# Kernel tuning notes

Measured on AMD Instinct MI355X. Metric: run time of the kernel, lower is better.

Reference implementation:

```python
import jax, jax.numpy as jnp
import numpy as np

LN_EPS = 1e-5
NORM_EPS = 1e-12
TEMPERATURE = 0.5


def _project(h, W1, b1, W2, b2, g, beta):
    # projection head: Linear -> ReLU -> Linear -> LayerNorm, then L2 normalize
    x = jnp.maximum(h @ W1 + b1, 0.0) @ W2 + b2          # [B, P]
    mu = jnp.mean(x, axis=-1, keepdims=True)
    var = jnp.mean(jnp.square(x - mu), axis=-1, keepdims=True)
    x = (x - mu) * jax.lax.rsqrt(var + LN_EPS) * g + beta
    n = jnp.linalg.norm(x, axis=-1, keepdims=True)
    return x / jnp.maximum(n, NORM_EPS)                   # [B, P]


def setup_inputs() -> dict:
    key = jax.random.key(0)
    ks = jax.random.split(key, 8)
    B, H, P, K, NBUF = 16384, 2048, 256, 64, 2000
    Hh = H // 2
    return {
        "hidden_states": jax.random.normal(ks[0], (B, H), jnp.float32),
        "positive_hidden": jax.random.normal(ks[1], (B, H), jnp.float32),
        "neg_buffer": jax.random.normal(ks[2], (NBUF, P), jnp.float32),
        "W1": jax.random.normal(ks[3], (H, Hh), jnp.float32) * (1.0 / np.sqrt(H)),
        "b1": jnp.zeros((Hh,), jnp.float32),
        "W2": jax.random.normal(ks[4], (Hh, P), jnp.float32) * (1.0 / np.sqrt(Hh)),
        "b2": jnp.zeros((P,), jnp.float32),
        "ln_gamma": jnp.ones((P,), jnp.float32),
        "ln_beta": jnp.zeros((P,), jnp.float32),
        "neg_indices": jax.random.randint(ks[5], (B, K), 0, NBUF, jnp.int32),
    }


def reference(hidden_states, positive_hidden, neg_buffer, W1, b1, W2, b2,
              ln_gamma, ln_beta, neg_indices):
    anchors = _project(hidden_states, W1, b1, W2, b2, ln_gamma, ln_beta)      # [B,P]
    positives = _project(positive_hidden, W1, b1, W2, b2, ln_gamma, ln_beta)  # [B,P]
    # negatives are detached in the original (buffer stores .detach() features)
    negs = jax.lax.stop_gradient(neg_buffer)[neg_indices]                      # [B,K,P]
    pos_sim = jnp.einsum('bp,bp->b', anchors, positives) / TEMPERATURE        # [B]
    neg_sims = jnp.einsum('bkp,bp->bk', negs, anchors) / TEMPERATURE          # [B,K]
    logits = jnp.concatenate([pos_sim[:, None], neg_sims], axis=1)            # [B,1+K]
    # cross-entropy with label 0 for every anchor, averaged over the batch
    loss = -jnp.mean(jax.nn.log_softmax(logits, axis=-1)[:, 0])
    return loss
```

## Files before the change

kernel.cpp:

```cpp
#include <hip/hip_runtime.h>
#include <hip/hip_bf16.h>
#include <cstdint>

#define BATCH   16384
#define HDIM    2048
#define HHDIM   1024
#define PDIM    256
#define KNEG    64
#define NBUF    2000
#define M1      (2 * BATCH)

typedef float  f32x4  __attribute__((ext_vector_type(4)));
typedef __bf16 bf16x8 __attribute__((ext_vector_type(8)));

typedef __attribute__((address_space(3))) unsigned int       lds_u32;
typedef __attribute__((address_space(1))) const unsigned int glb_u32;

__device__ __forceinline__ void gload_lds16(const void* g, void* l) {
  __builtin_amdgcn_global_load_lds((glb_u32*)g, (lds_u32*)l, 16, 0, 0);
}

#define VMCNT(n) asm volatile("s_waitcnt vmcnt(" #n ")" ::: "memory")

__global__ __launch_bounds__(256)
void cast_bf16_kernel(const float* __restrict__ src, __bf16* __restrict__ dst,
                      long n8) {
  long i = (long)blockIdx.x * blockDim.x + threadIdx.x;
  long stride = (long)gridDim.x * blockDim.x;
  for (; i < n8; i += stride) {
    f32x4 a = ((const f32x4*)src)[2 * i];
    f32x4 b = ((const f32x4*)src)[2 * i + 1];
    bf16x8 w;
    for (int j = 0; j < 4; ++j) { w[j] = (__bf16)a[j]; w[4 + j] = (__bf16)b[j]; }
    ((bf16x8*)dst)[i] = w;
  }
}

__global__ void transpose_cast_kernel(const float* __restrict__ src,
                                      __bf16* __restrict__ dst, int K, int N) {
  __shared__ float tile[32][33];
  int bn = blockIdx.x * 32, bk = blockIdx.y * 32;
  int tx = threadIdx.x, ty = threadIdx.y;
  for (int j = 0; j < 32; j += 8)
    tile[ty + j][tx] = src[(size_t)(bk + ty + j) * N + bn + tx];
  __syncthreads();
  for (int j = 0; j < 32; j += 8)
    dst[(size_t)(bn + ty + j) * K + bk + tx] = (__bf16)tile[tx][ty + j];
}

template <int KD, int BMH, int NBt, bool RELU_OUT, bool LNFUSE, int GRID>
__global__ __launch_bounds__(512)
void gemm_8ph(const __bf16* __restrict__ A, const __bf16* __restrict__ Bt,
              const float* __restrict__ bias,
              const float* __restrict__ lng, const float* __restrict__ lnb,
              void* __restrict__ Cv) {
  static_assert(!LNFUSE || NBt == 1, "LN fusion needs full rows per block");
  constexpr int KT    = KD / 64;
  constexpr int MI    = BMH / 32;
  constexpr int AHALF = BMH * 64;
  constexpr int BHALF = 128 * 64;
  constexpr int ASTEP = 2 * AHALF;
  constexpr int BSTEP = 2 * BHALF;
  constexpr int NDIM  = NBt * 256;
  constexpr int AUL   = BMH / 64;

  __shared__ __bf16 lA[2 * ASTEP];
  __shared__ __bf16 lB[2 * BSTEP];

  constexpr int Q = GRID / 8;
  int bid = blockIdx.x;
  int swb = (bid & 7) * Q + (bid >> 3);
  const int mb = swb / NBt, nb = swb % NBt;
  const long mrow0 = (long)mb * (2 * BMH);
  const int  ncol0 = nb * 256;

  const int tid = threadIdx.x;
  const int wid = tid >> 6, lane = tid & 63;
  const int wr = wid >> 2, wc = wid & 3;
  const int fl = lane & 15, fh = lane >> 4;

  int aoff[MI][2], boff[2][2];
  #pragma unroll
  for (int mi = 0; mi < MI; ++mi)
    #pragma unroll
    for (int ks = 0; ks < 2; ++ks) {
      int row = wr * (BMH / 2) + mi * 16 + fl;
      aoff[mi][ks] = row * 64 + (((ks * 4 + fh) ^ (row & 7)) * 8);
    }
  #pragma unroll
  for (int ni = 0; ni < 2; ++ni)
    #pragma unroll
    for (int ks = 0; ks < 2; ++ks) {
      int row = wc * 32 + ni * 16 + fl;
      boff[ni][ks] = row * 64 + (((ks * 4 + fh) ^ (row & 7)) * 8);
    }

  const int r0 = tid >> 3, sl = tid & 7;
  long aS[2][AUL], bS[2][2];
  #pragma unroll
  for (int h = 0; h < 2; ++h) {
    #pragma unroll
    for (int i = 0; i < AUL; ++i) {
      int rr = r0 + i * 64;
      int ss = sl ^ (rr & 7);
      aS[h][i] = (mrow0 + h * BMH + rr) * (long)KD + ss * 8;
    }
    #pragma unroll
    for (int i = 0; i < 2; ++i) {
      int rr = r0 + i * 64;
      int ss = sl ^ (rr & 7);
      bS[h][i] = ((long)(ncol0 + h * 128 + rr)) * KD + ss * 8;
    }
  }
  const int dstw = wid * 512;

  auto stA = [&](int h, int t) {
    __bf16* base = lA + (t & 1) * ASTEP + h * AHALF + dstw;
    #pragma unroll
    for (int i = 0; i < AUL; ++i)
      gload_lds16(A + aS[h][i] + (long)t * 64, (void*)(base + i * 4096));
  };
  auto stB = [&](int h, int t) {
    __bf16* base = lB + (t & 1) * BSTEP + h * BHALF + dstw;
    #pragma unroll
    for (int i = 0; i < 2; ++i)
      gload_lds16(Bt + bS[h][i] + (long)t * 64, (void*)(base + i * 4096));
  };

  bf16x8 aregA[MI][2], aregB[MI][2], breg0[2][2], breg1[2][2];
  auto loadA = [&](bf16x8 (&ar)[MI][2], int mh, int s) {
    const __bf16* base = lA + (s & 1) * ASTEP + mh * AHALF;
    #pragma unroll
    for (int mi = 0; mi < MI; ++mi)
      #pragma unroll
      for (int ks = 0; ks < 2; ++ks)
        ar[mi][ks] = *(const bf16x8*)(base + aoff[mi][ks]);
  };
  auto loadB = [&](bf16x8 (&br)[2][2], int nh, int s) {
    const __bf16* base = lB + (s & 1) * BSTEP + nh * BHALF;
    #pragma unroll
    for (int ni = 0; ni < 2; ++ni)
      #pragma unroll
      for (int ks = 0; ks < 2; ++ks)
        br[ni][ks] = *(const bf16x8*)(base + boff[ni][ks]);
  };

  f32x4 acc[2][2][MI][2] = {};

#define PHASE_MFMA(mh, nh, AR, BR)                                            \
  __builtin_amdgcn_s_setprio(1);                                              \
  _Pragma("unroll")                                                           \
  for (int ks = 0; ks < 2; ++ks) {                                            \
    _Pragma("unroll")                                                         \
    for (int mi = 0; mi < MI; ++mi) {                                         \
      _Pragma("unroll")                                                       \
      for (int ni = 0; ni < 2; ++ni)                                          \
        acc[mh][nh][mi][ni] = __builtin_amdgcn_mfma_f32_16x16x32_bf16(        \
            AR[mi][ks], BR[ni][ks], acc[mh][nh][mi][ni], 0, 0, 0);            \
    }                                                                         \
  }                                                                           \
  __builtin_amdgcn_s_setprio(0);

  stA(0, 0); stB(0, 0); stA(1, 0); stB(1, 0);
  stA(0, 1); stB(1, 1); stB(0, 1); stA(1, 1);
  if constexpr (AUL == 2) { VMCNT(8); } else { VMCNT(6); }
  __builtin_amdgcn_s_barrier();
  __builtin_amdgcn_sched_barrier(0);
  loadA(aregA, 0, 0);
  loadB(breg0, 0, 0);

  for (int s = 0; s < KT; ++s) {
    if (s >= 1 && s + 1 < KT) stB(0, s + 1);
    loadB(breg1, 1, s);
    PHASE_MFMA(0, 0, aregA, breg0);
    if (s + 1 < KT) {
      if constexpr (AUL == 2) { VMCNT(6); } else { VMCNT(5); }
    } else {
      VMCNT(0);
    }
    __builtin_amdgcn_s_barrier();
    __builtin_amdgcn_sched_barrier(0);

    if (s >= 1 && s + 1 < KT) stA(1, s + 1);
    loadA(aregB, 1, s);
    PHASE_MFMA(0, 1, aregA, breg1);
    __builtin_amdgcn_s_barrier();
    __builtin_amdgcn_sched_barrier(0);

    if (s + 2 < KT) stA(0, s + 2);
    PHASE_MFMA(1, 1, aregB, breg1);
    if (s + 2 < KT) {
      if constexpr (AUL == 2) { VMCNT(4); } else { VMCNT(2); }
    } else if (s + 1 < KT) {
      if constexpr (AUL == 2) { VMCNT(2); } else { VMCNT(1); }
    } else {
      VMCNT(0);
    }
    __builtin_amdgcn_s_barrier();
    __builtin_amdgcn_sched_barrier(0);

    if (s + 2 < KT) stB(1, s + 2);
    PHASE_MFMA(1, 0, aregB, breg0);
    if (s + 1 < KT) {
      loadA(aregA, 0, s + 1);
      loadB(breg0, 0, s + 1);
    }
    __builtin_amdgcn_s_barrier();
    __builtin_amdgcn_sched_barrier(0);
  }

#undef PHASE_MFMA

  if constexpr (LNFUSE) {
    float (*s1p)[4] = (float(*)[4])((float*)lA);
    float (*s2p)[4] = (float(*)[4])((float*)lA + 512);
    float (*n2p)[4] = (float(*)[4])((float*)lA + 1024);

    float v[2][2][MI][2][4];
    float gg[2][2], bb[2][2];
    #pragma unroll
    for (int nh = 0; nh < 2; ++nh)
      #pragma unroll
      for (int ni = 0; ni < 2; ++ni) {
        int c = nh * 128 + wc * 32 + ni * 16 + fl;
        float bv = bias[c];
        gg[nh][ni] = lng[c]; bb[nh][ni] = lnb[c];
        #pragma unroll
        for (int mh = 0; mh < 2; ++mh)
          #pragma unroll
          for (int mi = 0; mi < MI; ++mi)
            #pragma unroll
            for (int r = 0; r < 4; ++r)
              v[mh][nh][mi][ni][r] = acc[mh][nh][mi][ni][r] + bv;
      }

    #pragma unroll
    for (int mh = 0; mh < 2; ++mh)
      #pragma unroll
      for (int mi = 0; mi < MI; ++mi)
        #pragma unroll
        for (int r = 0; r < 4; ++r) {
          float s1 = 0.0f, s2 = 0.0f;
          #pragma unroll
          for (int nh = 0; nh < 2; ++nh)
            #pragma unroll
            for (int ni = 0; ni < 2; ++ni) {
              float x = v[mh][nh][mi][ni][r];
              s1 += x; s2 += x * x;
            }
          for (int m = 1; m < 16; m <<= 1) {
            s1 += __shfl_xor(s1, m, 64);
            s2 += __shfl_xor(s2, m, 64);
          }
          if (fl == 0) {
            int lr = mh * 64 + wr * 32 + mi * 16 + fh * 4 + r;
            s1p[lr][wc] = s1; s2p[lr][wc] = s2;
          }
        }
    __syncthreads();

    float n2loc[2][MI][4];
    #pragma unroll
    for (int mh = 0; mh < 2; ++mh)
      #pragma unroll
      for (int mi = 0; mi < MI; ++mi)
        #pragma unroll
        for (int r = 0; r < 4; ++r) {
          int lr = mh * 64 + wr * 32 + mi * 16 + fh * 4 + r;
          float t1 = s1p[lr][0] + s1p[lr][1] + s1p[lr][2] + s1p[lr][3];
          float t2 = s2p[lr][0] + s2p[lr][1] + s2p[lr][2] + s2p[lr][3];
          float mu = t1 * (1.0f / PDIM);
          float var = t2 * (1.0f / PDIM) - mu * mu;
          float rstd = rsqrtf(var + 1e-5f);
          float n2 = 0.0f;
          #pragma unroll
          for (int nh = 0; nh < 2; ++nh)
            #pragma unroll
            for (int ni = 0; ni < 2; ++ni) {
              float y = (v[mh][nh][mi][ni][r] - mu) * rstd * gg[nh][ni] + bb[nh][ni];
              v[mh][nh][mi][ni][r] = y;
              n2 += y * y;
            }
          for (int m = 1; m < 16; m <<= 1) n2 += __shfl_xor(n2, m, 64);
          n2loc[mh][mi][r] = n2;
        }
    #pragma unroll
    for (int mh = 0; mh < 2; ++mh)
      #pragma unroll
      for (int mi = 0; mi < MI; ++mi)
        #pragma unroll
        for (int r = 0; r < 4; ++r)
          if (fl == 0) {
            int lr = mh * 64 + wr * 32 + mi * 16 + fh * 4 + r;
            n2p[lr][wc] = n2loc[mh][mi][r];
          }
    __syncthreads();

    #pragma unroll
    for (int mh = 0; mh < 2; ++mh)
      #pragma unroll
      for (int mi = 0; mi < MI; ++mi)
        #pragma unroll
        for (int r = 0; r < 4; ++r) {
          int lr = mh * 64 + wr * 32 + mi * 16 + fh * 4 + r;
          float t = n2p[lr][0] + n2p[lr][1] + n2p[lr][2] + n2p[lr][3];
          float sc = 1.0f / fmaxf(sqrtf(t), 1e-12f);
          #pragma unroll
          for (int nh = 0; nh < 2; ++nh)
            #pragma unroll
            for (int ni = 0; ni < 2; ++ni) {
              int c = nh * 128 + wc * 32 + ni * 16 + fl;
              ((float*)Cv)[(mrow0 + lr) * NDIM + c] = v[mh][nh][mi][ni][r] * sc;
            }
        }
  } else {
    #pragma unroll
    for (int mh = 0; mh < 2; ++mh)
      #pragma unroll
      for (int nh = 0; nh < 2; ++nh)
        #pragma unroll
        for (int ni = 0; ni < 2; ++ni) {
          int col = ncol0 + nh * 128 + wc * 32 + ni * 16 + fl;
          float bv = bias[col];
          #pragma unroll
          for (int mi = 0; mi < MI; ++mi)
            #pragma unroll
            for (int r = 0; r < 4; ++r) {
              long row = mrow0 + mh * BMH + wr * (BMH / 2) + mi * 16 + fh * 4 + r;
              float x = acc[mh][nh][mi][ni][r] + bv;
              if constexpr (RELU_OUT) {
                x = fmaxf(x, 0.0f);
                ((__bf16*)Cv)[row * NDIM + col] = (__bf16)x;
              } else {
                ((float*)Cv)[row * NDIM + col] = x;
              }
            }
        }
  }
}

__global__ __launch_bounds__(256)
void loss_kernel(const float* __restrict__ X, const __bf16* __restrict__ negb,
                 const int* __restrict__ nidx, float* __restrict__ partials) {
  __shared__ float lsum[4];
  int b    = blockIdx.x * 4 + (threadIdx.x >> 6);
  int lane = threadIdx.x & 63;
  int g = lane >> 4, lg = lane & 15;

  const float* arow = X + (size_t)b * PDIM;
  const float* prow = X + (size_t)(BATCH + b) * PDIM;

  float a16[16];
  #pragma unroll
  for (int j = 0; j < 4; ++j) {
    f32x4 av = *(const f32x4*)(arow + lg * 16 + j * 4);
    #pragma unroll
    for (int e = 0; e < 4; ++e) a16[j * 4 + e] = av[e];
  }

  float ps = 0.0f;
  #pragma unroll
  for (int j = 0; j < 4; ++j) {
    f32x4 p = *(const f32x4*)(prow + lg * 16 + j * 4);
    #pragma unroll
    for (int e = 0; e < 4; ++e) ps += a16[j * 4 + e] * p[e];
  }
  for (int m = 1; m < 16; m <<= 1) ps += __shfl_xor(ps, m, 64);
  float pos = ps * 2.0f;

  float myneg = -3.0e38f;
  for (int k4 = 0; k4 < 16; ++k4) {
    int k = k4 * 4 + g;
    int idx = nidx[(size_t)b * KNEG + k];
    const __bf16* nrow = negb + (size_t)idx * PDIM;
    float sv = 0.0f;
    #pragma unroll
    for (int j = 0; j < 2; ++j) {
      bf16x8 nv = *(const bf16x8*)(nrow + lg * 16 + j * 8);
      #pragma unroll
      for (int e = 0; e < 8; ++e) sv += a16[j * 8 + e] * (float)nv[e];
    }
    for (int m = 1; m < 16; m <<= 1) sv += __shfl_xor(sv, m, 64);
    if (lg == k4) myneg = sv * 2.0f;
  }

  float mx = myneg;
  for (int m = 1; m < 64; m <<= 1) mx = fmaxf(mx, __shfl_xor(mx, m, 64));
  mx = fmaxf(mx, pos);
  float e = expf(myneg - mx);
  for (int m = 1; m < 64; m <<= 1) e += __shfl_xor(e, m, 64);
  float tot = e + expf(pos - mx);
  float lb = -(pos - mx - logf(tot));

  if (lane == 0) lsum[threadIdx.x >> 6] = lb;
  __syncthreads();
  if (threadIdx.x == 0)
    partials[blockIdx.x] = lsum[0] + lsum[1] + lsum[2] + lsum[3];
}

__global__ void finalize_kernel(const float* __restrict__ partials,
                                float* __restrict__ out) {
  __shared__ float ls[4];
  int tid = threadIdx.x;
  float s = 0.0f;
  for (int i = tid; i < 4096; i += 256) s += partials[i];
  for (int m = 1; m < 64; m <<= 1) s += __shfl_xor(s, m, 64);
  if ((tid & 63) == 0) ls[tid >> 6] = s;
  __syncthreads();
  if (tid == 0) out[0] = (ls[0] + ls[1] + ls[2] + ls[3]) * (1.0f / BATCH);
}

extern "C" void kernel_launch(void* const* d_in, const int* in_sizes, int n_in,
                              void* d_out, int out_size, void* d_ws, size_t ws_size,
                              hipStream_t stream) {
  const float* hidden   = (const float*)d_in[0];
  const float* positive = (const float*)d_in[1];
  const float* negbuf   = (const float*)d_in[2];
  const float* W1       = (const float*)d_in[3];
  const float* b1       = (const float*)d_in[4];
  const float* W2       = (const float*)d_in[5];
  const float* b2       = (const float*)d_in[6];
  const float* gamma    = (const float*)d_in[7];
  const float* beta     = (const float*)d_in[8];
  const int*   nidx     = (const int*)d_in[9];
  float* out = (float*)d_out;

  char* ws = (char*)d_ws;
  const size_t OFF_Y1   = 134217728;
  const size_t OFF_W1T  = OFF_Y1 + 67108864;
  const size_t OFF_W2T  = OFF_W1T + 4194304;
  const size_t OFF_NEGB = OFF_W2T + 524288;
  const size_t OFF_PART = OFF_NEGB + 1048576;

  __bf16* Abf      = (__bf16*)(ws);
  __bf16* Y1       = (__bf16*)(ws + OFF_Y1);
  __bf16* W1T      = (__bf16*)(ws + OFF_W1T);
  __bf16* W2T      = (__bf16*)(ws + OFF_W2T);
  __bf16* negb     = (__bf16*)(ws + OFF_NEGB);
  float*  partials = (float*) (ws + OFF_PART);
  float*  X        = (float*) (ws);

  transpose_cast_kernel<<<dim3(HHDIM / 32, HDIM / 32), dim3(32, 8), 0, stream>>>(
      W1, W1T, HDIM, HHDIM);
  transpose_cast_kernel<<<dim3(PDIM / 32, HHDIM / 32), dim3(32, 8), 0, stream>>>(
      W2, W2T, HHDIM, PDIM);

  const long n8 = (long)BATCH * HDIM / 8;
  cast_bf16_kernel<<<2048, 256, 0, stream>>>(hidden, Abf, n8);
  cast_bf16_kernel<<<2048, 256, 0, stream>>>(positive, Abf + (size_t)BATCH * HDIM, n8);
  cast_bf16_kernel<<<256, 256, 0, stream>>>(negbuf, negb, (long)NBUF * PDIM / 8);

  gemm_8ph<HDIM, 128, HHDIM / 256, true, false, (M1 / 256) * (HHDIM / 256)>
      <<<(M1 / 256) * (HHDIM / 256), 512, 0, stream>>>(
          Abf, W1T, b1, nullptr, nullptr, Y1);

  gemm_8ph<HHDIM, 64, PDIM / 256, false, true, (M1 / 128) * (PDIM / 256)>
      <<<(M1 / 128) * (PDIM / 256), 512, 0, stream>>>(
          Y1, W2T, b2, gamma, beta, X);

  loss_kernel<<<BATCH / 4, 256, 0, stream>>>(X, negb, nidx, partials);
  finalize_kernel<<<1, 256, 0, stream>>>(partials, out);
}
```

Baseline: 304.3 us.

## Replace first projection GEMM with smaller-tile triple-buffered kernel for higher occupancy

Adds a lighter GEMM kernel for the first projection layer. It uses a 128x256 tile, a K-step of 32 and three LDS buffers with a swizzled layout, and launch bounds that request four blocks per CU. The previous 8-phase kernel used a larger 256-row tile. The aim is to raise occupancy and overlap global-to-LDS loads with MFMA work. In exchange, each K-step does less work per barrier and the launch has twice as many blocks. The bias and ReLU epilogue writes scattered bf16 stores.

```diff
diff --git a/kernel.cpp b/kernel.cpp
--- a/kernel.cpp
+++ b/kernel.cpp
@@ -46,6 +46,107 @@
   __syncthreads();
   for (int j = 0; j < 32; j += 8)
     dst[(size_t)(bn + ty + j) * K + bk + tx] = (__bf16)tile[tx][ty + j];
+}
+
+template <int KD, int NBt, int GRID>
+__global__ __launch_bounds__(512, 4)
+void gemm_lite(const __bf16* __restrict__ A, const __bf16* __restrict__ Bt,
+               const float* __restrict__ bias, __bf16* __restrict__ C) {
+  constexpr int KT   = KD / 32;
+  constexpr int ABUF = 128 * 32;
+  constexpr int BBUF = 256 * 32;
+  constexpr int NDIM = NBt * 256;
+
+  __shared__ __bf16 lA[3 * ABUF];
+  __shared__ __bf16 lB[3 * BBUF];
+
+  constexpr int Q = GRID / 8;
+  int bid = blockIdx.x;
+  int swb = (bid & 7) * Q + (bid >> 3);
+  const int mb = swb / NBt, nb = swb % NBt;
+  const long mrow0 = (long)mb * 128;
+  const int  ncol0 = nb * 256;
+
+  const int tid = threadIdx.x;
+  const int wid = tid >> 6, lane = tid & 63;
+  const int wr = wid >> 2, wc = wid & 3;
+  const int fl = lane & 15, fh = lane >> 4;
+
+  int aoff[4], boff[4];
+  #pragma unroll
+  for (int mi = 0; mi < 4; ++mi) {
+    int row = wr * 64 + mi * 16 + fl;
+    aoff[mi] = row * 32 + ((fh ^ ((row >> 1) & 3)) * 8);
+  }
+  #pragma unroll
+  for (int ni = 0; ni < 4; ++ni) {
+    int row = wc * 64 + ni * 16 + fl;
+    boff[ni] = row * 32 + ((fh ^ ((row >> 1) & 3)) * 8);
+  }
+
+  const int r0 = tid >> 2, sl = tid & 3;
+  const long aS  = (mrow0 + r0) * (long)KD + ((sl ^ ((r0 >> 1) & 3)) * 8);
+  const long bS0 = ((long)(ncol0 + r0)) * KD + ((sl ^ ((r0 >> 1) & 3)) * 8);
+  const long bS1 = ((long)(ncol0 + r0 + 128)) * KD +
+                   ((sl ^ (((r0 + 128) >> 1) & 3)) * 8);
+  const int dstw = wid * 512;
+
+  auto stage = [&](int t, int bi) {
+    gload_lds16(A + aS + (long)t * 32, (void*)(lA + bi * ABUF + dstw));
+    gload_lds16(Bt + bS0 + (long)t * 32, (void*)(lB + bi * BBUF + dstw));
+    gload_lds16(Bt + bS1 + (long)t * 32, (void*)(lB + bi * BBUF + 4096 + dstw));
+  };
+
+  f32x4 acc[4][4] = {};
+
+  stage(0, 0);
+  stage(1, 1);
+  VMCNT(3);
+  __builtin_amdgcn_s_barrier();
+  __builtin_amdgcn_sched_barrier(0);
+
+  int cur = 0;
+  for (int s = 0; s < KT; ++s) {
+    const int stg = (cur >= 1) ? cur - 1 : 2;
+    if (s + 2 < KT) stage(s + 2, stg);
+
+    bf16x8 af[4], bf[4];
+    #pragma unroll
+    for (int mi = 0; mi < 4; ++mi)
+      af[mi] = *(const bf16x8*)(lA + cur * ABUF + aoff[mi]);
+    #pragma unroll
+    for (int ni = 0; ni < 4; ++ni)
+      bf[ni] = *(const bf16x8*)(lB + cur * BBUF + boff[ni]);
+
+    __builtin_amdgcn_s_setprio(1);
+    #pragma unroll
+    for (int mi = 0; mi < 4; ++mi)
+      #pragma unroll
+      for (int ni = 0; ni < 4; ++ni)
+        acc[mi][ni] = __builtin_amdgcn_mfma_f32_16x16x32_bf16(
+            af[mi], bf[ni], acc[mi][ni], 0, 0, 0);
+    __builtin_amdgcn_s_setprio(0);
+
+    if (s + 2 < KT)      { VMCNT(3); }
+    else if (s + 1 < KT) { VMCNT(0); }
+    __builtin_amdgcn_s_barrier();
+    __builtin_amdgcn_sched_barrier(0);
+    cur = (cur >= 2) ? 0 : cur + 1;
+  }
+
+  #pragma unroll
+  for (int ni = 0; ni < 4; ++ni) {
+    int col = ncol0 + wc * 64 + ni * 16 + fl;
+    float bv = bias[col];
+    #pragma unroll
+    for (int mi = 0; mi < 4; ++mi)
+      #pragma unroll
+      for (int r = 0; r < 4; ++r) {
+        long row = mrow0 + wr * 64 + mi * 16 + fh * 4 + r;
+        float v = fmaxf(acc[mi][ni][r] + bv, 0.0f);
+        C[row * NDIM + col] = (__bf16)v;
+      }
+  }
 }
 
 template <int KD, int BMH, int NBt, bool RELU_OUT, bool LNFUSE, int GRID>
@@ -450,9 +551,8 @@
   cast_bf16_kernel<<<2048, 256, 0, stream>>>(positive, Abf + (size_t)BATCH * HDIM, n8);
   cast_bf16_kernel<<<256, 256, 0, stream>>>(negbuf, negb, (long)NBUF * PDIM / 8);
 
-  gemm_8ph<HDIM, 128, HHDIM / 256, true, false, (M1 / 256) * (HHDIM / 256)>
-      <<<(M1 / 256) * (HHDIM / 256), 512, 0, stream>>>(
-          Abf, W1T, b1, nullptr, nullptr, Y1);
+  gemm_lite<HDIM, HHDIM / 256, (M1 / 128) * (HHDIM / 256)>
+      <<<(M1 / 128) * (HHDIM / 256), 512, 0, stream>>>(Abf, W1T, b1, Y1);
 
   gemm_8ph<HHDIM, 64, PDIM / 256, false, true, (M1 / 128) * (PDIM / 256)>
       <<<(M1 / 128) * (PDIM / 256), 512, 0, stream>>>(
```

Measured after the change: 326.8 us. +7.4%, slower.

## Fuse fp32-to-bf16 input cast into first projection GEMM

Applied to the files above, without the earlier changes.

Replaces the separate cast kernels for hidden and positive activations with a new GEMM that streams fp32 A tiles into LDS and converts them to bf16 in registers before the MFMAs. This removes a full write and re-read of the 128MB bf16 copy of the inputs. In exchange, the GEMM reads twice as many A bytes per tile, uses a K-step of 32 with a new 4-phase pipeline, and spends extra VALU work on conversion, which may lower MFMA utilisation.

```diff
diff --git a/kernel.cpp b/kernel.cpp
--- a/kernel.cpp
+++ b/kernel.cpp
@@ -21,6 +21,7 @@
 }
 
 #define VMCNT(n) asm volatile("s_waitcnt vmcnt(" #n ")" ::: "memory")
+#define LGKM(n)  asm volatile("s_waitcnt lgkmcnt(" #n ")" ::: "memory")
 
 __global__ __launch_bounds__(256)
 void cast_bf16_kernel(const float* __restrict__ src, __bf16* __restrict__ dst,
@@ -46,6 +47,168 @@
   __syncthreads();
   for (int j = 0; j < 32; j += 8)
     dst[(size_t)(bn + ty + j) * K + bk + tx] = (__bf16)tile[tx][ty + j];
+}
+
+template <int KD, int NBt, int GRID>
+__global__ __launch_bounds__(512)
+void gemm_f32a(const float* __restrict__ A0, const float* __restrict__ A1v,
+               const __bf16* __restrict__ Bt, const float* __restrict__ bias,
+               __bf16* __restrict__ C) {
+  constexpr int KT   = KD / 32;
+  constexpr int NDIM = NBt * 256;
+
+  __shared__ float  lAf[2 * 2 * 4096];
+  __shared__ __bf16 lBf[2 * 2 * 4096];
+
+  constexpr int Q = GRID / 8;
+  int bid = blockIdx.x;
+  int swb = (bid & 7) * Q + (bid >> 3);
+  const int mb = swb / NBt, nb = swb % NBt;
+  const long mrow0 = (long)mb * 256;
+  const int  ncol0 = nb * 256;
+
+  const float* Af = (mrow0 < BATCH) ? (A0 + mrow0 * (long)KD)
+                                    : (A1v + (mrow0 - BATCH) * (long)KD);
+
+  const int tid = threadIdx.x;
+  const int wid = tid >> 6, lane = tid & 63;
+  const int wr = wid >> 2, wc = wid & 3;
+  const int fl = lane & 15, fh = lane >> 4;
+
+  int aoffs[4][2];
+  #pragma unroll
+  for (int mi = 0; mi < 4; ++mi)
+    #pragma unroll
+    for (int p = 0; p < 2; ++p) {
+      int row = wr * 64 + mi * 16 + fl;
+      aoffs[mi][p] = row * 32 + (((2 * fh + p) ^ (row & 7)) * 4);
+    }
+  int boffs[2];
+  #pragma unroll
+  for (int ni = 0; ni < 2; ++ni) {
+    int row = wc * 32 + ni * 16 + fl;
+    boffs[ni] = row * 32 + ((fh ^ ((row >> 1) & 3)) * 8);
+  }
+
+  const int r0a = tid >> 3, ssa = (tid & 7) ^ ((tid >> 3) & 7);
+  const int r0b = tid >> 2, ssb = (tid & 3) ^ (((tid >> 2) >> 1) & 3);
+  const int dwA = wid * 256;
+  const int dwB = wid * 512;
+
+  auto stA = [&](int h, int t) {
+    float* base = lAf + (t & 1) * 8192 + h * 4096 + dwA;
+    const float* s0 = Af + (size_t)(h * 128 + r0a) * KD + t * 32 + ssa * 4;
+    gload_lds16(s0, (void*)base);
+    gload_lds16(s0 + (size_t)64 * KD, (void*)(base + 2048));
+  };
+  auto stB = [&](int h, int t) {
+    __bf16* base = lBf + (t & 1) * 8192 + h * 4096 + dwB;
+    gload_lds16(Bt + (size_t)(ncol0 + h * 128 + r0b) * KD + t * 32 + ssb * 8,
+                (void*)base);
+  };
+
+  f32x4  aA[4][2];
+  bf16x8 areg[4], breg0[2], breg1[2];
+
+  auto loadAraw = [&](int mh, int s) {
+    const float* base = lAf + (s & 1) * 8192 + mh * 4096;
+    #pragma unroll
+    for (int mi = 0; mi < 4; ++mi)
+      #pragma unroll
+      for (int p = 0; p < 2; ++p)
+        aA[mi][p] = *(const f32x4*)(base + aoffs[mi][p]);
+  };
+  auto cvtA = [&]() {
+    #pragma unroll
+    for (int mi = 0; mi < 4; ++mi)
+      #pragma unroll
+      for (int j = 0; j < 4; ++j) {
+        areg[mi][j]     = (__bf16)aA[mi][0][j];
+        areg[mi][4 + j] = (__bf16)aA[mi][1][j];
+      }
+  };
+  auto loadB = [&](bf16x8 (&br)[2], int nh, int s) {
+    const __bf16* base = lBf + (s & 1) * 8192 + nh * 4096;
+    #pragma unroll
+    for (int ni = 0; ni < 2; ++ni)
+      br[ni] = *(const bf16x8*)(base + boffs[ni]);
+  };
+
+  f32x4 acc[2][2][4][2] = {};
+
+#define QMFMA(mh, nh, BR)                                                     \
+  __builtin_amdgcn_s_setprio(1);                                              \
+  _Pragma("unroll")                                                           \
+  for (int mi = 0; mi < 4; ++mi) {                                            \
+    _Pragma("unroll")                                                         \
+    for (int ni = 0; ni < 2; ++ni)                                            \
+      acc[mh][nh][mi][ni] = __builtin_amdgcn_mfma_f32_16x16x32_bf16(          \
+          areg[mi], BR[ni], acc[mh][nh][mi][ni], 0, 0, 0);                    \
+  }                                                                           \
+  __builtin_amdgcn_s_setprio(0);
+
+  stA(0, 0); stB(0, 0); stA(1, 0); stB(1, 0);
+  stA(0, 1); stB(1, 1); stB(0, 1); stA(1, 1);
+  VMCNT(6);
+  __builtin_amdgcn_s_barrier();
+  __builtin_amdgcn_sched_barrier(0);
+
+  for (int s = 0; s < KT; ++s) {
+    loadAraw(0, s);
+    loadB(breg0, 0, s);
+    if (s >= 1 && s + 1 < KT) stB(0, s + 1);
+    __builtin_amdgcn_s_barrier();
+    LGKM(0);
+    __builtin_amdgcn_sched_barrier(0);
+    cvtA();
+    QMFMA(0, 0, breg0);
+    __builtin_amdgcn_s_barrier();
+
+    loadB(breg1, 1, s);
+    if (s >= 1 && s + 1 < KT) stA(1, s + 1);
+    __builtin_amdgcn_s_barrier();
+    LGKM(0);
+    __builtin_amdgcn_sched_barrier(0);
+    QMFMA(0, 1, breg1);
+    __builtin_amdgcn_s_barrier();
+
+    loadAraw(1, s);
+    if (s + 2 < KT) stA(0, s + 2);
+    __builtin_amdgcn_s_barrier();
+    LGKM(0);
+    __builtin_amdgcn_sched_barrier(0);
+    cvtA();
+    QMFMA(1, 1, breg1);
+    __builtin_amdgcn_s_barrier();
+
+    if (s + 2 < KT) stB(1, s + 2);
+    __builtin_amdgcn_s_barrier();
+    __builtin_amdgcn_sched_barrier(0);
+    QMFMA(1, 0, breg0);
+    if (s + 2 < KT) { VMCNT(3); } else { VMCNT(0); }
+    __builtin_amdgcn_s_barrier();
+    __builtin_amdgcn_sched_barrier(0);
+  }
+
+#undef QMFMA
+
+  #pragma unroll
+  for (int mh = 0; mh < 2; ++mh)
+    #pragma unroll
+    for (int nh = 0; nh < 2; ++nh)
+      #pragma unroll
+      for (int ni = 0; ni < 2; ++ni) {
+        int col = ncol0 + nh * 128 + wc * 32 + ni * 16 + fl;
+        float bv = bias[col];
+        #pragma unroll
+        for (int mi = 0; mi < 4; ++mi)
+          #pragma unroll
+          for (int r = 0; r < 4; ++r) {
+            long row = mrow0 + mh * 128 + wr * 64 + mi * 16 + fh * 4 + r;
+            float v = fmaxf(acc[mh][nh][mi][ni][r] + bv, 0.0f);
+            C[row * NDIM + col] = (__bf16)v;
+          }
+      }
 }
 
 template <int KD, int BMH, int NBt, bool RELU_OUT, bool LNFUSE, int GRID>
@@ -426,33 +589,28 @@
   float* out = (float*)d_out;
 
   char* ws = (char*)d_ws;
-  const size_t OFF_Y1   = 134217728;
-  const size_t OFF_W1T  = OFF_Y1 + 67108864;
+  const size_t OFF_W1T  = 67108864;
   const size_t OFF_W2T  = OFF_W1T + 4194304;
   const size_t OFF_NEGB = OFF_W2T + 524288;
   const size_t OFF_PART = OFF_NEGB + 1048576;
-
-  __bf16* Abf      = (__bf16*)(ws);
-  __bf16* Y1       = (__bf16*)(ws + OFF_Y1);
+  const size_t OFF_X    = OFF_PART + 16384;
+
+  __bf16* Y1       = (__bf16*)(ws);
   __bf16* W1T      = (__bf16*)(ws + OFF_W1T);
   __bf16* W2T      = (__bf16*)(ws + OFF_W2T);
   __bf16* negb     = (__bf16*)(ws + OFF_NEGB);
   float*  partials = (float*) (ws + OFF_PART);
-  float*  X        = (float*) (ws);
+  float*  X        = (float*) (ws + OFF_X);
 
   transpose_cast_kernel<<<dim3(HHDIM / 32, HDIM / 32), dim3(32, 8), 0, stream>>>(
       W1, W1T, HDIM, HHDIM);
   transpose_cast_kernel<<<dim3(PDIM / 32, HHDIM / 32), dim3(32, 8), 0, stream>>>(
       W2, W2T, HHDIM, PDIM);
-
-  const long n8 = (long)BATCH * HDIM / 8;
-  cast_bf16_kernel<<<2048, 256, 0, stream>>>(hidden, Abf, n8);
-  cast_bf16_kernel<<<2048, 256, 0, stream>>>(positive, Abf + (size_t)BATCH * HDIM, n8);
   cast_bf16_kernel<<<256, 256, 0, stream>>>(negbuf, negb, (long)NBUF * PDIM / 8);
 
-  gemm_8ph<HDIM, 128, HHDIM / 256, true, false, (M1 / 256) * (HHDIM / 256)>
+  gemm_f32a<HDIM, HHDIM / 256, (M1 / 256) * (HHDIM / 256)>
       <<<(M1 / 256) * (HHDIM / 256), 512, 0, stream>>>(
-          Abf, W1T, b1, nullptr, nullptr, Y1);
+          hidden, positive, W1T, b1, Y1);
 
   gemm_8ph<HHDIM, 64, PDIM / 256, false, true, (M1 / 128) * (PDIM / 256)>
       <<<(M1 / 128) * (PDIM / 256), 512, 0, stream>>>(
```

Result: no change. 308.1 us (+1.2%).
